# Kernel optimization log

Measured on AMD Instinct MI355X. Metric: run time of the kernel, lower is better.

Reference implementation:

```python
import jax, jax.numpy as jnp
import numpy as np

D = 2048  # input_dimensions (== seq_len, required by the module's math)
H = 8192  # hidden_dimensions
B = 4
S = D


def setup_inputs() -> dict:
    key = jax.random.key(0)
    ks = jax.random.split(key, 13)
    scale_in = 1.0 / np.sqrt(D)
    scale_hid = 1.0 / np.sqrt(H)
    def lin(k, fan_in, fan_out, s):
        return jax.random.normal(k, (fan_in, fan_out), jnp.float32) * s
    inp = {"x": jax.random.normal(ks[0], (B, S, D), jnp.float32)}
    names = ["q", "k", "v"]
    for i, n in enumerate(names):
        inp[f"{n}_w1"] = lin(ks[1 + 4 * i], D, H, scale_in)
        inp[f"{n}_b1"] = jnp.zeros((H,), jnp.float32)
        inp[f"{n}_w2"] = lin(ks[2 + 4 * i], H, D, scale_hid)
        inp[f"{n}_b2"] = jnp.zeros((D,), jnp.float32)
    return inp


def _mlp(x, w1, b1, w2, b2):
    # Linear(D,H) -> ReLU -> Linear(H,D)
    h = jax.nn.relu(jnp.einsum("bsd,dh->bsh", x, w1) + b1)
    return jnp.einsum("bsh,hd->bsd", h, w2) + b2


def reference(x, q_w1, q_b1, q_w2, q_b2, k_w1, k_b1, k_w2, k_b2,
              v_w1, v_b1, v_w2, v_b2):
    Q = _mlp(x, q_w1, q_b1, q_w2, q_b2)
    K = _mlp(x, k_w1, k_b1, k_w2, k_b2)
    V = _mlp(x, v_w1, v_b1, v_w2, v_b2)
    # scores: Q @ K^T  -> [B, S, S]  (no 1/sqrt(d) scaling in original)
    scores = jnp.einsum("bsd,btd->bst", Q, K)
    # nn.Softmax(dim=1): over axis 1 (rows), NOT the usual last axis
    probs = jax.nn.softmax(scores, axis=1)
    # original computes V @ probs (requires S == D)
    out = jnp.einsum("bsd,bdt->bst", V, probs)
    return out
```

## Files before the change

### kernel.cpp

```cpp
#include <hip/hip_runtime.h>
#include <cstdint>
#include <cstddef>

typedef __attribute__((ext_vector_type(8))) short short8;
typedef __attribute__((ext_vector_type(4))) short short4v;
typedef __attribute__((ext_vector_type(4))) float f32x4;
typedef __attribute__((ext_vector_type(4))) int i32x4;

#define DEV __device__ __forceinline__

constexpr int DD = 2048;
constexpr int HHID = 8192;
constexpr int BB = 4;
constexpr int SS = 2048;
constexpr size_t NX = (size_t)BB * SS * DD;
constexpr size_t NW = (size_t)DD * HHID;
constexpr size_t NH = (size_t)BB * SS * HHID;

constexpr size_t OFF_XH  = 0;
constexpr size_t OFF_XA1 = OFF_XH + NX * 2;
constexpr size_t OFF_XA2 = OFF_XA1 + NX;
constexpr size_t OFF_WA1 = OFF_XA2 + NX;
constexpr size_t OFF_WA2 = OFF_WA1 + NW;
constexpr size_t OFF_WHV = OFF_WA1;
constexpr size_t OFF_HH  = OFF_WA2 + NW;
constexpr size_t OFF_HL  = OFF_HH + NH * 2;
constexpr size_t OFF_QKH = OFF_HL + NH * 2;
constexpr size_t OFF_QKL = OFF_QKH + NX * 2;
constexpr size_t OFF_QA1 = OFF_QKL + NX * 2;
constexpr size_t OFF_QA2 = OFF_QA1 + NX;
constexpr size_t OFF_KA1 = OFF_QA2 + NX;
constexpr size_t OFF_KA2 = OFF_KA1 + NX;
constexpr size_t OFF_HA1 = OFF_KA2 + NX;
constexpr size_t OFF_HA2 = OFF_HA1 + NH;
constexpr size_t OFF_V   = OFF_HA2 + NH;
constexpr size_t OFF_XS  = OFF_V + NX * 2;
constexpr size_t OFF_HS  = OFF_XS + 32768;
constexpr size_t OFF_QS  = OFF_HS + 32768;
constexpr size_t OFF_KS  = OFF_QS + 32768;
constexpr size_t OFF_CM  = OFF_KS + 32768;
constexpr size_t WS_TOTAL = OFF_CM + 32768;
constexpr size_t OFF_ST = OFF_HH;
constexpr size_t OFF_PT = OFF_HL;

__device__ __align__(256) unsigned char g_ws[WS_TOTAL];

DEV unsigned char* wsbase(unsigned char* p) { return p ? p : (unsigned char*)g_ws; }
DEV short f2bf(float v) { __bf16 b = (__bf16)v; return __builtin_bit_cast(short, b); }
DEV float bf2f(short s) { return (float)__builtin_bit_cast(__bf16, s); }

template <typename T> DEV void nts(T v, T* p) { __builtin_nontemporal_store(v, p); }
template <typename T> DEV T ntl(const T* p) { return __builtin_nontemporal_load(p); }

DEV void gl16(const short* g, short* l) {
  __builtin_amdgcn_global_load_lds((const __attribute__((address_space(1))) void*)g,
                                   (__attribute__((address_space(3))) void*)l, 16, 0, 0);
}
DEV void gl16b(const signed char* g, signed char* l) {
  __builtin_amdgcn_global_load_lds((const __attribute__((address_space(1))) void*)g,
                                   (__attribute__((address_space(3))) void*)l, 16, 0, 0);
}

DEV void raster2d(int rem, int gx, int grp, int& by, int& bx) {
  const int tpg = grp * gx;
  const int gidx = rem / tpg;
  const int o = rem - gidx * tpg;
  const int r = o / grp;
  by = gidx * grp + (o - r * grp);
  bx = r;
}

__global__ void cast_hi_k(const float* __restrict__ x, unsigned char* wsb,
                          size_t oh, size_t n4) {
  unsigned char* ws = wsbase(wsb);
  short4v* OH = (short4v*)(ws + oh);
  const f32x4* X = (const f32x4*)x;
  for (size_t i = (size_t)blockIdx.x * blockDim.x + threadIdx.x; i < n4;
       i += (size_t)gridDim.x * blockDim.x) {
    const f32x4 v = ntl(&X[i]);
    short4v hs;
#pragma unroll
    for (int e = 0; e < 4; ++e) hs[e] = f2bf(v[e]);
    OH[i] = hs;
  }
}

__launch_bounds__(256)
__global__ void quant_x_k(const float* __restrict__ x, unsigned char* wsb,
                          size_t oa1, size_t oa2, size_t oxs) {
  unsigned char* ws = wsbase(wsb);
  signed char* A1 = (signed char*)(ws + oa1);
  signed char* A2 = (signed char*)(ws + oa2);
  float* XS = (float*)(ws + oxs);
  const int row = blockIdx.x;
  const float* xr = x + (size_t)row * 2048;
  const int tid = threadIdx.x, lane = tid & 63;
  const f32x4 v0 = *(const f32x4*)&xr[tid * 8];
  const f32x4 v1 = *(const f32x4*)&xr[tid * 8 + 4];
  float m = 0.0f;
#pragma unroll
  for (int e = 0; e < 4; ++e) m = fmaxf(m, fmaxf(fabsf(v0[e]), fabsf(v1[e])));
#pragma unroll
  for (int o = 32; o; o >>= 1) m = fmaxf(m, __shfl_xor(m, o));
  __shared__ float rb[4];
  if (lane == 0) rb[tid >> 6] = m;
  __syncthreads();
  m = fmaxf(fmaxf(rb[0], rb[1]), fmaxf(rb[2], rb[3]));
  const float inv = (m > 1e-30f) ? 127.0f / m : 0.0f;
  if (tid == 0) XS[row] = m * (1.0f / 127.0f);
  unsigned int w1a = 0, w1b = 0, w2a = 0, w2b = 0;
#pragma unroll
  for (int e = 0; e < 8; ++e) {
    const float xv = (e < 4) ? v0[e] : v1[e - 4];
    const float q = xv * inv;
    const float a1f = rintf(q);
    int ia2 = (int)rintf((q - a1f) * 256.0f);
    ia2 = ia2 > 127 ? 127 : (ia2 < -127 ? -127 : ia2);
    const unsigned int b1 = (unsigned char)(signed char)(int)a1f;
    const unsigned int b2 = (unsigned char)(signed char)ia2;
    if (e < 4) { w1a |= b1 << (8 * e); w2a |= b2 << (8 * e); }
    else       { w1b |= b1 << (8 * (e - 4)); w2b |= b2 << (8 * (e - 4)); }
  }
  const size_t o = (size_t)row * 2048 + tid * 8;
  *(unsigned int*)&A1[o] = w1a; *(unsigned int*)&A1[o + 4] = w1b;
  *(unsigned int*)&A2[o] = w2a; *(unsigned int*)&A2[o + 4] = w2b;
}

__launch_bounds__(1024)
__global__ void rowquant_k(unsigned char* wsb, size_t hho, size_t hlo,
                           size_t oa1, size_t oa2, size_t oso, int rowlen) {
  unsigned char* ws = wsbase(wsb);
  const int row = blockIdx.x, tid = threadIdx.x, lane = tid & 63, wv = tid >> 6;
  const int nw = blockDim.x >> 6;
  const short8 hi = ntl((const short8*)((const short*)(ws + hho) + (size_t)row * rowlen) + tid);
  const short8 lo = ntl((const short8*)((const short*)(ws + hlo) + (size_t)row * rowlen) + tid);
  float v[8]; float m = 0.0f;
#pragma unroll
  for (int e = 0; e < 8; ++e) {
    v[e] = bf2f(hi[e]) + bf2f(lo[e]);
    m = fmaxf(m, fabsf(v[e]));
  }
#pragma unroll
  for (int o = 32; o; o >>= 1) m = fmaxf(m, __shfl_xor(m, o));
  __shared__ float rb[16];
  if (lane == 0) rb[wv] = m;
  __syncthreads();
  m = rb[0];
  for (int i = 1; i < nw; ++i) m = fmaxf(m, rb[i]);
  const float inv = (m > 1e-30f) ? 127.0f / m : 0.0f;
  if (tid == 0) ((float*)(ws + oso))[row] = m * (1.0f / 127.0f);
  unsigned int w1a = 0, w1b = 0, w2a = 0, w2b = 0;
#pragma unroll
  for (int e = 0; e < 8; ++e) {
    const float q = v[e] * inv;
    const float a1f = rintf(q);
    int ia2 = (int)rintf((q - a1f) * 256.0f);
    ia2 = ia2 > 127 ? 127 : (ia2 < -127 ? -127 : ia2);
    const unsigned int b1 = (unsigned char)(signed char)(int)a1f;
    const unsigned int b2 = (unsigned char)(signed char)ia2;
    if (e < 4) { w1a |= b1 << (8 * e); w2a |= b2 << (8 * e); }
    else       { w1b |= b1 << (8 * (e - 4)); w2b |= b2 << (8 * (e - 4)); }
  }
  const size_t o = (size_t)row * rowlen + tid * 8;
  signed char* A1 = (signed char*)(ws + oa1);
  signed char* A2 = (signed char*)(ws + oa2);
  *(unsigned int*)&A1[o] = w1a; *(unsigned int*)&A1[o + 4] = w1b;
  *(unsigned int*)&A2[o] = w2a; *(unsigned int*)&A2[o + 4] = w2b;
}

__launch_bounds__(256)
__global__ void colmax_k(const float* __restrict__ w, unsigned char* wsb,
                         size_t omax, int R, int C) {
  unsigned char* ws = wsbase(wsb);
  unsigned int* MX = (unsigned int*)(ws + omax);
  const int col = blockIdx.x * 256 + threadIdx.x;
  const int r0 = blockIdx.y * 128;
  float m = 0.0f;
  for (int r = 0; r < 128; ++r) m = fmaxf(m, fabsf(w[(size_t)(r0 + r) * C + col]));
  atomicMax(&MX[col], __float_as_uint(m));
}

__global__ void scalefix_k(unsigned char* wsb, size_t off, int n) {
  unsigned char* ws = wsbase(wsb);
  const int i = blockIdx.x * 256 + threadIdx.x;
  if (i < n) {
    float* p = (float*)(ws + off);
    const unsigned int u = ((const unsigned int*)p)[i];
    p[i] = __uint_as_float(u) * (1.0f / 127.0f);
  }
}

__global__ void transpose_quant_k(const float* __restrict__ src, unsigned char* wsb,
                                  size_t oa1, size_t oa2, size_t osc, int R, int C) {
  __shared__ float t[32][33];
  unsigned char* ws = wsbase(wsb);
  signed char* A1 = (signed char*)(ws + oa1);
  signed char* A2 = (signed char*)(ws + oa2);
  const float* SC = (const float*)(ws + osc);
  const int c0 = blockIdx.x << 5, r0 = blockIdx.y << 5;
  const int x = threadIdx.x, y = threadIdx.y;
#pragma unroll
  for (int i = 0; i < 4; ++i) {
    const int rr = y + (i << 3);
    t[rr][x] = ntl(&src[(size_t)(r0 + rr) * C + c0 + x]);
  }
  __syncthreads();
#pragma unroll
  for (int i = 0; i < 4; ++i) {
    const int oc = y + (i << 3);
    const float v = t[x][oc];
    const float s = SC[c0 + oc];
    const float inv = (s > 1e-38f) ? 1.0f / s : 0.0f;
    const float q = v * inv;
    const float a1f = rintf(q);
    int ia2 = (int)rintf((q - a1f) * 256.0f);
    ia2 = ia2 > 127 ? 127 : (ia2 < -127 ? -127 : ia2);
    const size_t o = (size_t)(c0 + oc) * R + r0 + x;
    A1[o] = (signed char)(int)a1f;
    A2[o] = (signed char)ia2;
  }
}

__global__ void transpose_cast_k(const float* __restrict__ src, unsigned char* wsb,
                                 size_t oh, int R, int C) {
  __shared__ float t[32][33];
  unsigned char* ws = wsbase(wsb);
  short* OH = (short*)(ws + oh);
  const int c0 = blockIdx.x << 5, r0 = blockIdx.y << 5;
  const int x = threadIdx.x, y = threadIdx.y;
#pragma unroll
  for (int i = 0; i < 4; ++i) {
    const int rr = y + (i << 3);
    t[rr][x] = ntl(&src[(size_t)(r0 + rr) * C + c0 + x]);
  }
  __syncthreads();
#pragma unroll
  for (int i = 0; i < 4; ++i) {
    const int oc = y + (i << 3);
    OH[(size_t)(c0 + oc) * R + r0 + x] = f2bf(t[x][oc]);
  }
}

DEV i32x4 mfma_i8(i32x4 a, i32x4 b, i32x4 c) {
  return __builtin_amdgcn_mfma_i32_16x16x64_i8(a, b, c, 0, 0, 0);
}
DEV i32x4 rfi8(const signed char* base, int lstride, int L, int row, int fg) {
  return *(const i32x4*)&base[L * lstride + row * 64 + ((fg ^ ((row >> 1) & 3)) << 4)];
}

template <bool RELU, int STORE>
__launch_bounds__(512, 2)
__global__ void gemm_i8_k(unsigned char* wsb,
                          size_t a1o, size_t a2o, size_t b1o, size_t b2o,
                          size_t aso, size_t bso, const float* __restrict__ bias,
                          size_t o0, size_t o1, int M, int N, int K,
                          int gx, int gxy, int grp) {
  __shared__ alignas(16) signed char lds8[114688];

  unsigned char* ws = wsbase(wsb);
  const int tid = threadIdx.x;
  const int lane = tid & 63;
  const int wave = tid >> 6;
  const int wm = (wave >> 2) << 6;
  const int wn = (wave & 3) << 6;
  const int fr = lane & 15;
  const int fg = lane >> 4;

  const int nwg = gridDim.x;
  const int q8 = nwg >> 3;
  const int id = (blockIdx.x & 7) * q8 + (blockIdx.x >> 3);
  const int bz = id / gxy;
  const int rem = id - bz * gxy;
  int by, bx;
  raster2d(rem, gx, grp, by, bx);
  const int brow = by << 7;
  const int bcol = bx << 8;

  const size_t batchA = (size_t)bz * M * K;
  const size_t batchB = (STORE == 2) ? (size_t)bz * N * K : 0;
  const signed char* Xa1 = (const signed char*)(ws + a1o) + batchA;
  const signed char* Xa2 = (const signed char*)(ws + a2o) + batchA;
  const signed char* Wa1 = (const signed char*)(ws + b1o) + batchB;
  const signed char* Wa2 = (const signed char*)(ws + b2o) + batchB;
  const float* AS = (const float*)(ws + aso) + (size_t)bz * M;
  const float* BS = (const float*)(ws + bso) + ((STORE == 2) ? (size_t)bz * N : 0);

  const int ar = tid >> 2, ac = tid & 3;
  const size_t aOff = (size_t)(brow + ar) * K + ((ac ^ ((ar >> 1) & 3)) << 4);
  size_t bOff[2];
#pragma unroll
  for (int h = 0; h < 2; ++h) {
    const int G = tid + h * 512;
    const int r = G >> 2, c = G & 3;
    bOff[h] = (size_t)(bcol + r) * K + ((c ^ ((r >> 1) & 3)) << 4);
  }

  auto stageA = [&](int slotBase, int tt) {
    const int ko = tt * 64;
    gl16b(Xa1 + aOff + ko, &lds8[slotBase + (tid << 4)]);
    gl16b(Xa2 + aOff + ko, &lds8[slotBase + 8192 + (tid << 4)]);
  };
  auto stageB = [&](int slotBase, int tt) {
    const int ko = tt * 64;
#pragma unroll
    for (int h = 0; h < 2; ++h) {
      gl16b(Wa1 + bOff[h] + ko, &lds8[slotBase + ((tid + h * 512) << 4)]);
      gl16b(Wa2 + bOff[h] + ko, &lds8[slotBase + 16384 + ((tid + h * 512) << 4)]);
    }
  };

  const int nt = K / 64;
  i32x4 I1[4][4] = {};
  i32x4 I2[4][4] = {};

  stageA(0, 0);
  stageB(49152, 0);
  if (nt > 1) { stageA(16384, 1); stageB(49152 + 32768, 1); }
  if (nt > 1) { asm volatile("s_waitcnt vmcnt(6)" ::: "memory"); }
  else        { asm volatile("s_waitcnt vmcnt(0)" ::: "memory"); }
  __builtin_amdgcn_s_barrier();

  for (int t = 0; t < nt; ++t) {
    const signed char* aS = &lds8[(t % 3) * 16384];
    const signed char* bS = &lds8[49152 + (t & 1) * 32768];
    const int sA2 = ((t + 2) % 3) * 16384;
    const int sB2 = 49152 + (t & 1) * 32768;
    const bool pf = (t + 2 < nt);
    i32x4 bf[4][2], af[2][2];

    if (pf) stageA(sA2, t + 2);
#pragma unroll
    for (int j = 0; j < 4; ++j) {
      bf[j][0] = rfi8(bS, 16384, 0, wn + j * 16 + fr, fg);
      bf[j][1] = rfi8(bS, 16384, 1, wn + j * 16 + fr, fg);
    }
#pragma unroll
    for (int i = 0; i < 2; ++i) {
      af[i][0] = rfi8(aS, 8192, 0, wm + i * 16 + fr, fg);
      af[i][1] = rfi8(aS, 8192, 1, wm + i * 16 + fr, fg);
    }
    __builtin_amdgcn_s_setprio(1);
#pragma unroll
    for (int i = 0; i < 2; ++i)
#pragma unroll
      for (int j = 0; j < 4; ++j) {
        I1[i][j] = mfma_i8(af[i][0], bf[j][0], I1[i][j]);
        I2[i][j] = mfma_i8(af[i][0], bf[j][1], I2[i][j]);
        I2[i][j] = mfma_i8(af[i][1], bf[j][0], I2[i][j]);
      }
    __builtin_amdgcn_s_setprio(0);
    __builtin_amdgcn_s_barrier();

    asm volatile("" ::: "memory");
    if (pf) stageB(sB2, t + 2);
#pragma unroll
    for (int i = 0; i < 2; ++i) {
      af[i][0] = rfi8(aS, 8192, 0, wm + (2 + i) * 16 + fr, fg);
      af[i][1] = rfi8(aS, 8192, 1, wm + (2 + i) * 16 + fr, fg);
    }
    __builtin_amdgcn_s_setprio(1);
#pragma unroll
    for (int i = 0; i < 2; ++i)
#pragma unroll
      for (int j = 0; j < 4; ++j) {
        I1[2 + i][j] = mfma_i8(af[i][0], bf[j][0], I1[2 + i][j]);
        I2[2 + i][j] = mfma_i8(af[i][0], bf[j][1], I2[2 + i][j]);
        I2[2 + i][j] = mfma_i8(af[i][1], bf[j][0], I2[2 + i][j]);
      }
    __builtin_amdgcn_s_setprio(0);
    if (pf) { asm volatile("s_waitcnt vmcnt(6)" ::: "memory"); }
    else    { asm volatile("s_waitcnt vmcnt(0)" ::: "memory"); }
    __builtin_amdgcn_s_barrier();
  }

  const int fq4 = fg << 2;
  if constexpr (STORE == 0) {
    short* ldsS = (short*)lds8;
    short* Oh = (short*)(ws + o0);
    short* Ol = (short*)(ws + o1);
#pragma unroll
    for (int rd = 0; rd < 2; ++rd) {
      __builtin_amdgcn_s_barrier();
#pragma unroll
      for (int i = 0; i < 4; ++i) {
        const int rl = wm + i * 16 + fq4;
        const f32x4 sa4 = *(const f32x4*)&AS[brow + rl];
#pragma unroll
        for (int j = 0; j < 4; ++j) {
          const int cl = wn + j * 16 + fr;
          const float sb = BS[bcol + cl];
          const float bv = bias ? bias[bcol + cl] : 0.0f;
#pragma unroll
          for (int e = 0; e < 4; ++e) {
            float u = ((float)I1[i][j][e] + (float)I2[i][j][e] * (1.0f / 256.0f)) *
                          (sa4[e] * sb) + bv;
            if (RELU) u = fmaxf(u, 0.0f);
            short v;
            if (rd == 0) {
              v = f2bf(u);
            } else {
              const short hb = f2bf(u);
              v = f2bf(u - bf2f(hb));
            }
            ldsS[(rl + e) * 264 + cl] = v;
          }
        }
      }
      __builtin_amdgcn_s_barrier();
      short* gout = (rd == 0) ? Oh : Ol;
#pragma unroll
      for (int gi = 0; gi < 8; ++gi) {
        const int g = gi * 512 + tid;
        const int row = g >> 5, cg = g & 31;
        const short8 v = *(const short8*)&ldsS[row * 264 + cg * 8];
        nts(v, (short8*)&gout[(size_t)(brow + row) * N + bcol + cg * 8]);
      }
    }
  } else {
    float* Of = (float*)(ws + o0) + (size_t)bz * M * N;
    float* ldsf = (float*)lds8;
#pragma unroll
    for (int h2 = 0; h2 < 2; ++h2) {
      __builtin_amdgcn_s_barrier();
      if ((wn >> 7) == h2) {
#pragma unroll
        for (int i = 0; i < 4; ++i) {
          const int rl = wm + i * 16 + fq4;
          const f32x4 sa4 = *(const f32x4*)&AS[brow + rl];
#pragma unroll
          for (int j = 0; j < 4; ++j) {
            const int cp = (wn & 127) + j * 16 + fr;
            const float sb = BS[bcol + wn + j * 16 + fr];
            f32x4 u;
#pragma unroll
            for (int e = 0; e < 4; ++e)
              u[e] = ((float)I1[i][j][e] + (float)I2[i][j][e] * (1.0f / 256.0f)) *
                     (sa4[e] * sb);
            *(f32x4*)&ldsf[cp * 132 + rl] = u;
          }
        }
      }
      __builtin_amdgcn_s_barrier();
#pragma unroll
      for (int gi = 0; gi < 8; ++gi) {
        const int g = gi * 512 + tid;
        const int tr = g >> 5, tc4 = (g & 31) << 2;
        const f32x4 v = *(const f32x4*)&ldsf[tr * 132 + tc4];
        nts(v, (f32x4*)&Of[(size_t)(bcol + h2 * 128 + tr) * M + brow + tc4]);
      }
    }
  }
}

constexpr int CH = 8192;

DEV short8 read_frag1(const short* base, int row, int s, int fg) {
  return *(const short8*)&base[row * 64 + ((((s << 2) | fg) ^ (row & 7)) << 3)];
}

DEV f32x4 mfma16(short8 a, short8 b, f32x4 c) {
  return __builtin_amdgcn_mfma_f32_16x16x32_bf16(a, b, c, 0, 0, 0);
}

template <bool RELU, int STORE>
__launch_bounds__(512, 2)
__global__ void gemm8_k(unsigned char* wsb,
                        size_t aoff0, size_t boff0,
                        const float* __restrict__ bias,
                        size_t ooff0, float* __restrict__ optr,
                        int M, int N, int K, int gx, int gxy, int grp) {
  __shared__ alignas(16) short lds[10 * CH];

  unsigned char* ws = wsbase(wsb);
  const int tid = threadIdx.x;
  const int lane = tid & 63;
  const int wave = tid >> 6;
  const int wm = (wave >> 2) << 7;
  const int wn = (wave & 3) << 6;

  const int nwg = gridDim.x;
  const int q8 = nwg >> 3;
  const int id = (blockIdx.x & 7) * q8 + (blockIdx.x >> 3);
  const int bz = id / gxy;
  const int rem = id - bz * gxy;
  int by, bx;
  raster2d(rem, gx, grp, by, bx);
  const int brow = by << 8;
  const int bcol = bx << 8;

  const short* A0 = (const short*)(ws + aoff0) + (size_t)bz * M * K;
  const short* B0g = (const short*)(ws + boff0) + (size_t)bz * N * K;

  size_t aSrc[2][2], bSrc[2][2];
#pragma unroll
  for (int h = 0; h < 2; ++h) {
    const int G = tid + h * 512;
    const int r = G >> 3, c = G & 7;
#pragma unroll
    for (int qq = 0; qq < 2; ++qq) {
      aSrc[qq][h] = (size_t)(brow + qq * 128 + r) * K + (size_t)((c ^ (r & 7)) << 3);
      bSrc[qq][h] = (size_t)(bcol + qq * 128 + r) * K + (size_t)((c ^ (r & 7)) << 3);
    }
  }
  const int ldst0 = tid << 3;

  auto issueA = [&](int slot, int qq, int tt) {
    short* dst = &lds[slot + qq * CH];
    const size_t ka = (size_t)tt * 64;
    gl16(A0 + aSrc[qq][0] + ka, dst + ldst0);
    gl16(A0 + aSrc[qq][1] + ka, dst + ldst0 + CH / 2);
  };
  auto issueB = [&](int slot, int qq, int tt) {
    short* dst = &lds[slot + qq * CH];
    const size_t ka = (size_t)tt * 64;
    gl16(B0g + bSrc[qq][0] + ka, dst + ldst0);
    gl16(B0g + bSrc[qq][1] + ka, dst + ldst0 + CH / 2);
  };

  const int nt = K / 64;
  const int fr = lane & 15;
  const int fg = lane >> 4;

  f32x4 acc[8][4] = {};

  issueA(0, 0, 0); issueA(0, 1, 0);
  issueB(6 * CH, 0, 0); issueB(6 * CH, 1, 0);
  if (nt > 1) {
    issueA(2 * CH, 0, 1); issueA(2 * CH, 1, 1);
    issueB(8 * CH, 0, 1); issueB(8 * CH, 1, 1);
    asm volatile("s_waitcnt vmcnt(8)" ::: "memory");
  } else {
    asm volatile("s_waitcnt vmcnt(0)" ::: "memory");
  }
  __builtin_amdgcn_s_barrier();

  for (int t = 0; t < nt; ++t) {
    const short* aBase = &lds[(t % 3) * (2 * CH)];
    const short* bBase = &lds[6 * CH + (t & 1) * (2 * CH)];
    const int sA2 = ((t + 2) % 3) * (2 * CH);
    const int sB  = 6 * CH + (t & 1) * (2 * CH);
    const bool pf = (t + 2 < nt);
    short8 bfr[4][2], av[4][2];

    if (pf) { issueA(sA2, 0, t + 2); issueA(sA2, 1, t + 2); }
#pragma unroll
    for (int j = 0; j < 4; ++j) {
      bfr[j][0] = read_frag1(bBase, wn + j * 16 + fr, 0, fg);
      bfr[j][1] = read_frag1(bBase, wn + j * 16 + fr, 1, fg);
    }
#pragma unroll
    for (int i = 0; i < 4; ++i) {
      av[i][0] = read_frag1(aBase, wm + i * 16 + fr, 0, fg);
      av[i][1] = read_frag1(aBase, wm + i * 16 + fr, 1, fg);
    }
    __builtin_amdgcn_s_setprio(1);
#pragma unroll
    for (int i = 0; i < 4; ++i)
#pragma unroll
      for (int j = 0; j < 4; ++j) {
        acc[i][j] = mfma16(av[i][0], bfr[j][0], acc[i][j]);
        acc[i][j] = mfma16(av[i][1], bfr[j][1], acc[i][j]);
      }
    __builtin_amdgcn_s_setprio(0);
    __builtin_amdgcn_s_barrier();

    asm volatile("" ::: "memory");
    if (pf) { issueB(sB, 0, t + 2); issueB(sB, 1, t + 2); }
#pragma unroll
    for (int i = 0; i < 4; ++i) {
      av[i][0] = read_frag1(aBase, wm + 64 + i * 16 + fr, 0, fg);
      av[i][1] = read_frag1(aBase, wm + 64 + i * 16 + fr, 1, fg);
    }
    __builtin_amdgcn_s_setprio(1);
#pragma unroll
    for (int i = 0; i < 4; ++i)
#pragma unroll
      for (int j = 0; j < 4; ++j) {
        acc[4 + i][j] = mfma16(av[i][0], bfr[j][0], acc[4 + i][j]);
        acc[4 + i][j] = mfma16(av[i][1], bfr[j][1], acc[4 + i][j]);
      }
    __builtin_amdgcn_s_setprio(0);
    if (pf) {
      asm volatile("s_waitcnt vmcnt(8)" ::: "memory");
    } else {
      asm volatile("s_waitcnt vmcnt(0)" ::: "memory");
    }
    __builtin_amdgcn_s_barrier();
  }

  const int fq4 = (lane >> 4) << 2;
  if constexpr (STORE == 1) {
    short* Oh = (short*)(ws + ooff0);
    __builtin_amdgcn_s_barrier();
#pragma unroll
    for (int i = 0; i < 8; ++i) {
      const int rl = wm + i * 16 + fq4;
#pragma unroll
      for (int j = 0; j < 4; ++j) {
        const int cl = wn + j * 16 + fr;
        const float bv = bias ? bias[bcol + cl] : 0.0f;
#pragma unroll
        for (int e = 0; e < 4; ++e) {
          float u = acc[i][j][e] + bv;
          if (RELU) u = fmaxf(u, 0.0f);
          lds[(rl + e) * 264 + cl] = f2bf(u);
        }
      }
    }
    __builtin_amdgcn_s_barrier();
#pragma unroll
    for (int gi = 0; gi < 16; ++gi) {
      const int g = gi * 512 + tid;
      const int row = g >> 5, cg = g & 31;
      const short8 v = *(const short8*)&lds[row * 264 + cg * 8];
      nts(v, (short8*)&Oh[(size_t)(brow + row) * N + bcol + cg * 8]);
    }
  } else {
    float* Op = optr + (size_t)bz * M * N;
    float* ldsf = (float*)lds;
#pragma unroll
    for (int h = 0; h < 2; ++h) {
      __builtin_amdgcn_s_barrier();
      if ((wm & 128) == (h << 7)) {
#pragma unroll
        for (int i = 0; i < 8; ++i) {
          const int rp = (wm & 127) + i * 16 + fq4;
#pragma unroll
          for (int j = 0; j < 4; ++j) {
            const int cl = wn + j * 16 + fr;
#pragma unroll
            for (int e = 0; e < 4; ++e)
              ldsf[(rp + e) * 258 + cl] = acc[i][j][e];
          }
        }
      }
      __builtin_amdgcn_s_barrier();
#pragma unroll
      for (int gi = 0; gi < 16; ++gi) {
        const int g = gi * 512 + tid;
        const int tr = g >> 6, tc4 = (g & 63) << 2;
        const f32x4 v = *(const f32x4*)&ldsf[tr * 258 + tc4];
        nts(v, (f32x4*)&Op[(size_t)(brow + h * 128 + tr) * N + bcol + tc4]);
      }
    }
  }
}

__launch_bounds__(256)
__global__ void softmax_rows_k(unsigned char* wsb, size_t st, size_t pt) {
  constexpr int S = 2048;
  unsigned char* ws = wsbase(wsb);
  const f32x4* row = (const f32x4*)((const float*)(ws + st) + (size_t)blockIdx.x * S);
  short4v* out = (short4v*)((short*)(ws + pt) + (size_t)blockIdx.x * S);
  const int tid = threadIdx.x, lane = tid & 63, wv = tid >> 6;
  const f32x4 a = ntl(&row[tid]);
  const f32x4 b = ntl(&row[tid + 256]);
  float m = fmaxf(fmaxf(fmaxf(a[0], a[1]), fmaxf(a[2], a[3])),
                  fmaxf(fmaxf(b[0], b[1]), fmaxf(b[2], b[3])));
#pragma unroll
  for (int o = 32; o; o >>= 1) m = fmaxf(m, __shfl_xor(m, o));
  __shared__ float rb[8];
  if (lane == 0) rb[wv] = m;
  __syncthreads();
  m = fmaxf(fmaxf(rb[0], rb[1]), fmaxf(rb[2], rb[3]));
  float e[8];
  float s = 0.0f;
#pragma unroll
  for (int q = 0; q < 4; ++q) { e[q] = expf(a[q] - m); s += e[q]; }
#pragma unroll
  for (int q = 0; q < 4; ++q) { e[4 + q] = expf(b[q] - m); s += e[4 + q]; }
#pragma unroll
  for (int o = 32; o; o >>= 1) s += __shfl_xor(s, o);
  if (lane == 0) rb[4 + wv] = s;
  __syncthreads();
  s = rb[4] + rb[5] + rb[6] + rb[7];
  const float inv = 1.0f / s;
  short4v o1, o2;
#pragma unroll
  for (int q = 0; q < 4; ++q) { o1[q] = f2bf(e[q] * inv); o2[q] = f2bf(e[4 + q] * inv); }
  nts(o1, &out[tid]);
  nts(o2, &out[tid + 256]);
}

extern "C" void kernel_launch(void* const* d_in, const int* in_sizes, int n_in,
                              void* d_out, int out_size, void* d_ws, size_t ws_size,
                              hipStream_t stream) {
  const float* x   = (const float*)d_in[0];
  const float* qw1 = (const float*)d_in[1];
  const float* qb1 = (const float*)d_in[2];
  const float* qw2 = (const float*)d_in[3];
  const float* qb2 = (const float*)d_in[4];
  const float* kw1 = (const float*)d_in[5];
  const float* kb1 = (const float*)d_in[6];
  const float* kw2 = (const float*)d_in[7];
  const float* kb2 = (const float*)d_in[8];
  const float* vw1 = (const float*)d_in[9];
  const float* vb1 = (const float*)d_in[10];
  const float* vw2 = (const float*)d_in[11];
  const float* vb2 = (const float*)d_in[12];
  float* out = (float*)d_out;
  unsigned char* wsb = (ws_size >= WS_TOTAL) ? (unsigned char*)d_ws : nullptr;
  unsigned char* wsr;
  if (wsb) wsr = wsb;
  else { hipError_t e = hipGetSymbolAddress((void**)&wsr, HIP_SYMBOL(g_ws)); (void)e; }

  const int M = BB * SS;
  dim3 blk(512);
  dim3 tb(32, 8);

  quant_x_k<<<8192, 256, 0, stream>>>(x, wsb, OFF_XA1, OFF_XA2, OFF_XS);
  cast_hi_k<<<4096, 256, 0, stream>>>(x, wsb, OFF_XH, NX / 4);

  hipMemsetAsync(wsr + OFF_CM, 0, 32768, stream);
  colmax_k<<<dim3(HHID / 256, DD / 128), 256, 0, stream>>>(qw1, wsb, OFF_CM, DD, HHID);
  scalefix_k<<<32, 256, 0, stream>>>(wsb, OFF_CM, HHID);
  transpose_quant_k<<<dim3(HHID / 32, DD / 32), tb, 0, stream>>>(qw1, wsb, OFF_WA1, OFF_WA2, OFF_CM, DD, HHID);
  gemm_i8_k<true, 0><<<2048, blk, 0, stream>>>(wsb, OFF_XA1, OFF_XA2, OFF_WA1, OFF_WA2,
                                               OFF_XS, OFF_CM, qb1, OFF_HH, OFF_HL,
                                               M, HHID, DD, 32, 2048, 8);
  rowquant_k<<<8192, 1024, 0, stream>>>(wsb, OFF_HH, OFF_HL, OFF_HA1, OFF_HA2, OFF_HS, HHID);
  hipMemsetAsync(wsr + OFF_CM, 0, 32768, stream);
  colmax_k<<<dim3(DD / 256, HHID / 128), 256, 0, stream>>>(qw2, wsb, OFF_CM, HHID, DD);
  scalefix_k<<<8, 256, 0, stream>>>(wsb, OFF_CM, DD);
  transpose_quant_k<<<dim3(DD / 32, HHID / 32), tb, 0, stream>>>(qw2, wsb, OFF_WA1, OFF_WA2, OFF_CM, HHID, DD);
  gemm_i8_k<false, 0><<<512, blk, 0, stream>>>(wsb, OFF_HA1, OFF_HA2, OFF_WA1, OFF_WA2,
                                               OFF_HS, OFF_CM, qb2, OFF_QKH, OFF_QKL,
                                               M, DD, HHID, 8, 512, 8);
  rowquant_k<<<8192, 256, 0, stream>>>(wsb, OFF_QKH, OFF_QKL, OFF_QA1, OFF_QA2, OFF_QS, DD);

  hipMemsetAsync(wsr + OFF_CM, 0, 32768, stream);
  colmax_k<<<dim3(HHID / 256, DD / 128), 256, 0, stream>>>(kw1, wsb, OFF_CM, DD, HHID);
  scalefix_k<<<32, 256, 0, stream>>>(wsb, OFF_CM, HHID);
  transpose_quant_k<<<dim3(HHID / 32, DD / 32), tb, 0, stream>>>(kw1, wsb, OFF_WA1, OFF_WA2, OFF_CM, DD, HHID);
  gemm_i8_k<true, 0><<<2048, blk, 0, stream>>>(wsb, OFF_XA1, OFF_XA2, OFF_WA1, OFF_WA2,
                                               OFF_XS, OFF_CM, kb1, OFF_HH, OFF_HL,
                                               M, HHID, DD, 32, 2048, 8);
  rowquant_k<<<8192, 1024, 0, stream>>>(wsb, OFF_HH, OFF_HL, OFF_HA1, OFF_HA2, OFF_HS, HHID);
  hipMemsetAsync(wsr + OFF_CM, 0, 32768, stream);
  colmax_k<<<dim3(DD / 256, HHID / 128), 256, 0, stream>>>(kw2, wsb, OFF_CM, HHID, DD);
  scalefix_k<<<8, 256, 0, stream>>>(wsb, OFF_CM, DD);
  transpose_quant_k<<<dim3(DD / 32, HHID / 32), tb, 0, stream>>>(kw2, wsb, OFF_WA1, OFF_WA2, OFF_CM, HHID, DD);
  gemm_i8_k<false, 0><<<512, blk, 0, stream>>>(wsb, OFF_HA1, OFF_HA2, OFF_WA1, OFF_WA2,
                                               OFF_HS, OFF_CM, kb2, OFF_QKH, OFF_QKL,
                                               M, DD, HHID, 8, 512, 8);
  rowquant_k<<<8192, 256, 0, stream>>>(wsb, OFF_QKH, OFF_QKL, OFF_KA1, OFF_KA2, OFF_KS, DD);

  transpose_cast_k<<<dim3(HHID / 32, DD / 32), tb, 0, stream>>>(vw1, wsb, OFF_WHV, DD, HHID);
  gemm8_k<true, 1><<<1024, blk, 0, stream>>>(
      wsb, OFF_XH, OFF_WHV, vb1, OFF_HH, nullptr, M, HHID, DD, 32, 1024, 4);
  transpose_cast_k<<<dim3(DD / 32, HHID / 32), tb, 0, stream>>>(vw2, wsb, OFF_WHV, HHID, DD);
  gemm8_k<false, 1><<<256, blk, 0, stream>>>(
      wsb, OFF_HH, OFF_WHV, vb2, OFF_V, nullptr, M, DD, HHID, 8, 256, 4);

  gemm_i8_k<false, 2><<<512, blk, 0, stream>>>(wsb, OFF_QA1, OFF_QA2, OFF_KA1, OFF_KA2,
                                               OFF_QS, OFF_KS, nullptr, OFF_ST, 0,
                                               SS, SS, DD, 8, 128, 8);

  softmax_rows_k<<<BB * SS, 256, 0, stream>>>(wsb, OFF_ST, OFF_PT);

  gemm8_k<false, 3><<<256, blk, 0, stream>>>(
      wsb, OFF_V, OFF_PT, nullptr, 0, out, SS, SS, DD, 8, 64, 4);
}
```

Before: 2.672 ms.

## Shrink int8 GEMM tile to 128x128 with 256-thread blocks

The split-int8 GEMM kernel moves from a 128x256 tile with 8 waves to a 128x128 tile with 4 waves. LDS staging, wait counts, epilogue strides and grid sizes are adjusted to match, and twice as many workgroups are launched. The aim is more concurrent blocks per CU (less LDS per block) and better load balance. The cost is lower operand reuse per tile and more global traffic for the A operand.

```diff
diff --git a/kernel.cpp b/kernel.cpp
--- a/kernel.cpp
+++ b/kernel.cpp
@@ -244,25 +244,25 @@
 DEV i32x4 mfma_i8(i32x4 a, i32x4 b, i32x4 c) {
   return __builtin_amdgcn_mfma_i32_16x16x64_i8(a, b, c, 0, 0, 0);
 }
-DEV i32x4 rfi8(const signed char* base, int lstride, int L, int row, int fg) {
-  return *(const i32x4*)&base[L * lstride + row * 64 + ((fg ^ ((row >> 1) & 3)) << 4)];
+DEV i32x4 rfi8(const signed char* base, int L, int row, int fg) {
+  return *(const i32x4*)&base[L * 8192 + row * 64 + ((fg ^ ((row >> 1) & 3)) << 4)];
 }
 
 template <bool RELU, int STORE>
-__launch_bounds__(512, 2)
+__launch_bounds__(256, 2)
 __global__ void gemm_i8_k(unsigned char* wsb,
                           size_t a1o, size_t a2o, size_t b1o, size_t b2o,
                           size_t aso, size_t bso, const float* __restrict__ bias,
                           size_t o0, size_t o1, int M, int N, int K,
                           int gx, int gxy, int grp) {
-  __shared__ alignas(16) signed char lds8[114688];
+  __shared__ alignas(16) signed char lds8[81920];
 
   unsigned char* ws = wsbase(wsb);
   const int tid = threadIdx.x;
   const int lane = tid & 63;
   const int wave = tid >> 6;
-  const int wm = (wave >> 2) << 6;
-  const int wn = (wave & 3) << 6;
+  const int wm = (wave >> 1) << 6;
+  const int wn = (wave & 1) << 6;
   const int fr = lane & 15;
   const int fg = lane >> 4;
 
@@ -274,7 +274,7 @@
   int by, bx;
   raster2d(rem, gx, grp, by, bx);
   const int brow = by << 7;
-  const int bcol = bx << 8;
+  const int bcol = bx << 7;
 
   const size_t batchA = (size_t)bz * M * K;
   const size_t batchB = (STORE == 2) ? (size_t)bz * N * K : 0;
@@ -285,27 +285,30 @@
   const float* AS = (const float*)(ws + aso) + (size_t)bz * M;
   const float* BS = (const float*)(ws + bso) + ((STORE == 2) ? (size_t)bz * N : 0);
 
-  const int ar = tid >> 2, ac = tid & 3;
-  const size_t aOff = (size_t)(brow + ar) * K + ((ac ^ ((ar >> 1) & 3)) << 4);
-  size_t bOff[2];
+  size_t aOff[2], bOff[2];
 #pragma unroll
   for (int h = 0; h < 2; ++h) {
-    const int G = tid + h * 512;
-    const int r = G >> 2, c = G & 3;
-    bOff[h] = (size_t)(bcol + r) * K + ((c ^ ((r >> 1) & 3)) << 4);
+    const int r = (tid >> 2) + h * 64;
+    const int c = tid & 3;
+    const int sw = (c ^ ((r >> 1) & 3)) << 4;
+    aOff[h] = (size_t)(brow + r) * K + sw;
+    bOff[h] = (size_t)(bcol + r) * K + sw;
   }
 
   auto stageA = [&](int slotBase, int tt) {
     const int ko = tt * 64;
-    gl16b(Xa1 + aOff + ko, &lds8[slotBase + (tid << 4)]);
-    gl16b(Xa2 + aOff + ko, &lds8[slotBase + 8192 + (tid << 4)]);
+#pragma unroll
+    for (int h = 0; h < 2; ++h) {
+      gl16b(Xa1 + aOff[h] + ko, &lds8[slotBase + ((tid + h * 256) << 4)]);
+      gl16b(Xa2 + aOff[h] + ko, &lds8[slotBase + 8192 + ((tid + h * 256) << 4)]);
+    }
   };
   auto stageB = [&](int slotBase, int tt) {
     const int ko = tt * 64;
 #pragma unroll
     for (int h = 0; h < 2; ++h) {
-      gl16b(Wa1 + bOff[h] + ko, &lds8[slotBase + ((tid + h * 512) << 4)]);
-      gl16b(Wa2 + bOff[h] + ko, &lds8[slotBase + 16384 + ((tid + h * 512) << 4)]);
+      gl16b(Wa1 + bOff[h] + ko, &lds8[slotBase + ((tid + h * 256) << 4)]);
+      gl16b(Wa2 + bOff[h] + ko, &lds8[slotBase + 8192 + ((tid + h * 256) << 4)]);
     }
   };
 
@@ -315,29 +318,29 @@
 
   stageA(0, 0);
   stageB(49152, 0);
-  if (nt > 1) { stageA(16384, 1); stageB(49152 + 32768, 1); }
-  if (nt > 1) { asm volatile("s_waitcnt vmcnt(6)" ::: "memory"); }
+  if (nt > 1) { stageA(16384, 1); stageB(65536, 1); }
+  if (nt > 1) { asm volatile("s_waitcnt vmcnt(8)" ::: "memory"); }
   else        { asm volatile("s_waitcnt vmcnt(0)" ::: "memory"); }
   __builtin_amdgcn_s_barrier();
 
   for (int t = 0; t < nt; ++t) {
     const signed char* aS = &lds8[(t % 3) * 16384];
-    const signed char* bS = &lds8[49152 + (t & 1) * 32768];
+    const signed char* bS = &lds8[49152 + (t & 1) * 16384];
     const int sA2 = ((t + 2) % 3) * 16384;
-    const int sB2 = 49152 + (t & 1) * 32768;
+    const int sB2 = 49152 + (t & 1) * 16384;
     const bool pf = (t + 2 < nt);
     i32x4 bf[4][2], af[2][2];
 
     if (pf) stageA(sA2, t + 2);
 #pragma unroll
     for (int j = 0; j < 4; ++j) {
-      bf[j][0] = rfi8(bS, 16384, 0, wn + j * 16 + fr, fg);
-      bf[j][1] = rfi8(bS, 16384, 1, wn + j * 16 + fr, fg);
+      bf[j][0] = rfi8(bS, 0, wn + j * 16 + fr, fg);
+      bf[j][1] = rfi8(bS, 1, wn + j * 16 + fr, fg);
     }
 #pragma unroll
     for (int i = 0; i < 2; ++i) {
-      af[i][0] = rfi8(aS, 8192, 0, wm + i * 16 + fr, fg);
-      af[i][1] = rfi8(aS, 8192, 1, wm + i * 16 + fr, fg);
+      af[i][0] = rfi8(aS, 0, wm + i * 16 + fr, fg);
+      af[i][1] = rfi8(aS, 1, wm + i * 16 + fr, fg);
     }
     __builtin_amdgcn_s_setprio(1);
 #pragma unroll
@@ -355,8 +358,8 @@
     if (pf) stageB(sB2, t + 2);
 #pragma unroll
     for (int i = 0; i < 2; ++i) {
-      af[i][0] = rfi8(aS, 8192, 0, wm + (2 + i) * 16 + fr, fg);
-      af[i][1] = rfi8(aS, 8192, 1, wm + (2 + i) * 16 + fr, fg);
+      af[i][0] = rfi8(aS, 0, wm + (2 + i) * 16 + fr, fg);
+      af[i][1] = rfi8(aS, 1, wm + (2 + i) * 16 + fr, fg);
     }
     __builtin_amdgcn_s_setprio(1);
 #pragma unroll
@@ -368,7 +371,7 @@
         I2[2 + i][j] = mfma_i8(af[i][1], bf[j][0], I2[2 + i][j]);
       }
     __builtin_amdgcn_s_setprio(0);
-    if (pf) { asm volatile("s_waitcnt vmcnt(6)" ::: "memory"); }
+    if (pf) { asm volatile("s_waitcnt vmcnt(8)" ::: "memory"); }
     else    { asm volatile("s_waitcnt vmcnt(0)" ::: "memory"); }
     __builtin_amdgcn_s_barrier();
   }
@@ -402,7 +405,7 @@
               const short hb = f2bf(u);
               v = f2bf(u - bf2f(hb));
             }
-            ldsS[(rl + e) * 264 + cl] = v;
+            ldsS[(rl + e) * 136 + cl] = v;
           }
         }
       }
@@ -410,44 +413,39 @@
       short* gout = (rd == 0) ? Oh : Ol;
 #pragma unroll
       for (int gi = 0; gi < 8; ++gi) {
-        const int g = gi * 512 + tid;
-        const int row = g >> 5, cg = g & 31;
-        const short8 v = *(const short8*)&ldsS[row * 264 + cg * 8];
+        const int g = gi * 256 + tid;
+        const int row = g >> 4, cg = g & 15;
+        const short8 v = *(const short8*)&ldsS[row * 136 + cg * 8];
         nts(v, (short8*)&gout[(size_t)(brow + row) * N + bcol + cg * 8]);
       }
     }
   } else {
     float* Of = (float*)(ws + o0) + (size_t)bz * M * N;
     float* ldsf = (float*)lds8;
-#pragma unroll
-    for (int h2 = 0; h2 < 2; ++h2) {
-      __builtin_amdgcn_s_barrier();
-      if ((wn >> 7) == h2) {
-#pragma unroll
-        for (int i = 0; i < 4; ++i) {
-          const int rl = wm + i * 16 + fq4;
-          const f32x4 sa4 = *(const f32x4*)&AS[brow + rl];
-#pragma unroll
-          for (int j = 0; j < 4; ++j) {
-            const int cp = (wn & 127) + j * 16 + fr;
-            const float sb = BS[bcol + wn + j * 16 + fr];
-            f32x4 u;
-#pragma unroll
-            for (int e = 0; e < 4; ++e)
-              u[e] = ((float)I1[i][j][e] + (float)I2[i][j][e] * (1.0f / 256.0f)) *
-                     (sa4[e] * sb);
-            *(f32x4*)&ldsf[cp * 132 + rl] = u;
-          }
-        }
-      }
-      __builtin_amdgcn_s_barrier();
-#pragma unroll
-      for (int gi = 0; gi < 8; ++gi) {
-        const int g = gi * 512 + tid;
-        const int tr = g >> 5, tc4 = (g & 31) << 2;
-        const f32x4 v = *(const f32x4*)&ldsf[tr * 132 + tc4];
-        nts(v, (f32x4*)&Of[(size_t)(bcol + h2 * 128 + tr) * M + brow + tc4]);
-      }
+    __builtin_amdgcn_s_barrier();
+#pragma unroll
+    for (int i = 0; i < 4; ++i) {
+      const int rbase = wm + i * 16 + fq4;
+      const f32x4 sa4 = *(const f32x4*)&AS[brow + rbase];
+#pragma unroll
+      for (int j = 0; j < 4; ++j) {
+        const int cp = wn + j * 16 + fr;
+        const float sb = BS[bcol + cp];
+        f32x4 u;
+#pragma unroll
+        for (int e = 0; e < 4; ++e)
+          u[e] = ((float)I1[i][j][e] + (float)I2[i][j][e] * (1.0f / 256.0f)) *
+                 (sa4[e] * sb);
+        *(f32x4*)&ldsf[cp * 132 + rbase] = u;
+      }
+    }
+    __builtin_amdgcn_s_barrier();
+#pragma unroll
+    for (int gi = 0; gi < 16; ++gi) {
+      const int g = gi * 256 + tid;
+      const int tr = g >> 5, tc4 = (g & 31) << 2;
+      const f32x4 v = *(const f32x4*)&ldsf[tr * 132 + tc4];
+      nts(v, (f32x4*)&Of[(size_t)(bcol + tr) * M + brow + tc4]);
     }
   }
 }
@@ -705,7 +703,8 @@
   else { hipError_t e = hipGetSymbolAddress((void**)&wsr, HIP_SYMBOL(g_ws)); (void)e; }
 
   const int M = BB * SS;
-  dim3 blk(512);
+  dim3 blk256(256);
+  dim3 blk512(512);
   dim3 tb(32, 8);
 
   quant_x_k<<<8192, 256, 0, stream>>>(x, wsb, OFF_XA1, OFF_XA2, OFF_XS);
@@ -715,49 +714,49 @@
   colmax_k<<<dim3(HHID / 256, DD / 128), 256, 0, stream>>>(qw1, wsb, OFF_CM, DD, HHID);
   scalefix_k<<<32, 256, 0, stream>>>(wsb, OFF_CM, HHID);
   transpose_quant_k<<<dim3(HHID / 32, DD / 32), tb, 0, stream>>>(qw1, wsb, OFF_WA1, OFF_WA2, OFF_CM, DD, HHID);
-  gemm_i8_k<true, 0><<<2048, blk, 0, stream>>>(wsb, OFF_XA1, OFF_XA2, OFF_WA1, OFF_WA2,
-                                               OFF_XS, OFF_CM, qb1, OFF_HH, OFF_HL,
-                                               M, HHID, DD, 32, 2048, 8);
+  gemm_i8_k<true, 0><<<4096, blk256, 0, stream>>>(wsb, OFF_XA1, OFF_XA2, OFF_WA1, OFF_WA2,
+                                                  OFF_XS, OFF_CM, qb1, OFF_HH, OFF_HL,
+                                                  M, HHID, DD, 64, 4096, 8);
   rowquant_k<<<8192, 1024, 0, stream>>>(wsb, OFF_HH, OFF_HL, OFF_HA1, OFF_HA2, OFF_HS, HHID);
   hipMemsetAsync(wsr + OFF_CM, 0, 32768, stream);
   colmax_k<<<dim3(DD / 256, HHID / 128), 256, 0, stream>>>(qw2, wsb, OFF_CM, HHID, DD);
   scalefix_k<<<8, 256, 0, stream>>>(wsb, OFF_CM, DD);
   transpose_quant_k<<<dim3(DD / 32, HHID / 32), tb, 0, stream>>>(qw2, wsb, OFF_WA1, OFF_WA2, OFF_CM, HHID, DD);
-  gemm_i8_k<false, 0><<<512, blk, 0, stream>>>(wsb, OFF_HA1, OFF_HA2, OFF_WA1, OFF_WA2,
-                                               OFF_HS, OFF_CM, qb2, OFF_QKH, OFF_QKL,
-                                               M, DD, HHID, 8, 512, 8);
+  gemm_i8_k<false, 0><<<1024, blk256, 0, stream>>>(wsb, OFF_HA1, OFF_HA2, OFF_WA1, OFF_WA2,
+                                                   OFF_HS, OFF_CM, qb2, OFF_QKH, OFF_QKL,
+                                                   M, DD, HHID, 16, 1024, 8);
   rowquant_k<<<8192, 256, 0, stream>>>(wsb, OFF_QKH, OFF_QKL, OFF_QA1, OFF_QA2, OFF_QS, DD);
 
   hipMemsetAsync(wsr + OFF_CM, 0, 32768, stream);
   colmax_k<<<dim3(HHID / 256, DD / 128), 256, 0, stream>>>(kw1, wsb, OFF_CM, DD, HHID);
   scalefix_k<<<32, 256, 0, stream>>>(wsb, OFF_CM, HHID);
   transpose_quant_k<<<dim3(HHID / 32, DD / 32), tb, 0, stream>>>(kw1, wsb, OFF_WA1, OFF_WA2, OFF_CM, DD, HHID);
-  gemm_i8_k<true, 0><<<2048, blk, 0, stream>>>(wsb, OFF_XA1, OFF_XA2, OFF_WA1, OFF_WA2,
-                                               OFF_XS, OFF_CM, kb1, OFF_HH, OFF_HL,
-                                               M, HHID, DD, 32, 2048, 8);
+  gemm_i8_k<true, 0><<<4096, blk256, 0, stream>>>(wsb, OFF_XA1, OFF_XA2, OFF_WA1, OFF_WA2,
+                                                  OFF_XS, OFF_CM, kb1, OFF_HH, OFF_HL,
+                                                  M, HHID, DD, 64, 4096, 8);
   rowquant_k<<<8192, 1024, 0, stream>>>(wsb, OFF_HH, OFF_HL, OFF_HA1, OFF_HA2, OFF_HS, HHID);
   hipMemsetAsync(wsr + OFF_CM, 0, 32768, stream);
   colmax_k<<<dim3(DD / 256, HHID / 128), 256, 0, stream>>>(kw2, wsb, OFF_CM, HHID, DD);
   scalefix_k<<<8, 256, 0, stream>>>(wsb, OFF_CM, DD);
   transpose_quant_k<<<dim3(DD / 32, HHID / 32), tb, 0, stream>>>(kw2, wsb, OFF_WA1, OFF_WA2, OFF_CM, HHID, DD);
-  gemm_i8_k<false, 0><<<512, blk, 0, stream>>>(wsb, OFF_HA1, OFF_HA2, OFF_WA1, OFF_WA2,
-                                               OFF_HS, OFF_CM, kb2, OFF_QKH, OFF_QKL,
-                                               M, DD, HHID, 8, 512, 8);
+  gemm_i8_k<false, 0><<<1024, blk256, 0, stream>>>(wsb, OFF_HA1, OFF_HA2, OFF_WA1, OFF_WA2,
+                                                   OFF_HS, OFF_CM, kb2, OFF_QKH, OFF_QKL,
+                                                   M, DD, HHID, 16, 1024, 8);
   rowquant_k<<<8192, 256, 0, stream>>>(wsb, OFF_QKH, OFF_QKL, OFF_KA1, OFF_KA2, OFF_KS, DD);
 
   transpose_cast_k<<<dim3(HHID / 32, DD / 32), tb, 0, stream>>>(vw1, wsb, OFF_WHV, DD, HHID);
-  gemm8_k<true, 1><<<1024, blk, 0, stream>>>(
+  gemm8_k<true, 1><<<1024, blk512, 0, stream>>>(
       wsb, OFF_XH, OFF_WHV, vb1, OFF_HH, nullptr, M, HHID, DD, 32, 1024, 4);
   transpose_cast_k<<<dim3(DD / 32, HHID / 32), tb, 0, stream>>>(vw2, wsb, OFF_WHV, HHID, DD);
-  gemm8_k<false, 1><<<256, blk, 0, stream>>>(
+  gemm8_k<false, 1><<<256, blk512, 0, stream>>>(
       wsb, OFF_HH, OFF_WHV, vb2, OFF_V, nullptr, M, DD, HHID, 8, 256, 4);
 
-  gemm_i8_k<false, 2><<<512, blk, 0, stream>>>(wsb, OFF_QA1, OFF_QA2, OFF_KA1, OFF_KA2,
-                                               OFF_QS, OFF_KS, nullptr, OFF_ST, 0,
-                                               SS, SS, DD, 8, 128, 8);
+  gemm_i8_k<false, 2><<<1024, blk256, 0, stream>>>(wsb, OFF_QA1, OFF_QA2, OFF_KA1, OFF_KA2,
+                                                   OFF_QS, OFF_KS, nullptr, OFF_ST, 0,
+                                                   SS, SS, DD, 16, 256, 8);
 
   softmax_rows_k<<<BB * SS, 256, 0, stream>>>(wsb, OFF_ST, OFF_PT);
 
-  gemm8_k<false, 3><<<256, blk, 0, stream>>>(
+  gemm8_k<false, 3><<<256, blk512, 0, stream>>>(
       wsb, OFF_V, OFF_PT, nullptr, 0, out, SS, SS, DD, 8, 64, 4);
 }
```

Result: no change. 2.716 ms (+1.7%).
